# Optimization experiments

Measured on AMD Instinct MI355X. Metric: run time of the kernel, lower is better.

Reference implementation:

```python
import jax, jax.numpy as jnp
import numpy as np

N, D_IN, D_OUT = 8192, 4096, 4096
ACT_BITS = 8


def setup_inputs() -> dict:
    key = jax.random.key(0)
    k1, k2, k3 = jax.random.split(key, 3)
    x = jax.random.normal(k1, (N, D_IN), dtype=jnp.float32)
    # ternary weight buffer in {-1, 0, +1} (stored as int8 in torch; int32 here)
    weight = jax.random.randint(k2, (D_OUT, D_IN), -1, 2, dtype=jnp.int32)
    weight_scale = jnp.array(0.05, dtype=jnp.float32)
    bias = jax.random.normal(k3, (D_OUT,), dtype=jnp.float32) * 0.01
    return {"x": x, "weight": weight, "weight_scale": weight_scale, "bias": bias}


def reference(x, weight, weight_scale, bias):
    qmax = 2.0 ** (ACT_BITS - 1) - 1.0   # 127
    qmin = -(2.0 ** (ACT_BITS - 1))      # -128
    # absmax activation quantization (eval-mode path of the module)
    scale = jnp.max(jnp.abs(x)) / qmax
    scale = jnp.where(scale == 0, jnp.float32(1.0), scale)
    x_int = jnp.clip(jnp.round(x / scale), qmin, qmax)
    # ternary matmul: pos_mask - neg_mask == weight itself for ternary values,
    # so F.linear(x, pos) - F.linear(x, neg) == x @ W^T
    w = weight.astype(jnp.float32)
    out = x_int @ w.T  # [N, D_OUT]
    out = out * weight_scale * scale
    return out + bias
```

## Files before the change

kernel.cpp:

```cpp
#include <hip/hip_runtime.h>
#include <hip/hip_bf16.h>

#define M_DIM 8192
#define N_DIM 4096
#define K_DIM 4096

typedef __attribute__((ext_vector_type(4))) int int4v;

__device__ __forceinline__ int quant4(float4 v, float rs) {
    float r0 = rintf(v.x * rs), r1 = rintf(v.y * rs);
    float r2 = rintf(v.z * rs), r3 = rintf(v.w * rs);
    int i0 = (int)fminf(127.0f, fmaxf(-128.0f, r0));
    int i1 = (int)fminf(127.0f, fmaxf(-128.0f, r1));
    int i2 = (int)fminf(127.0f, fmaxf(-128.0f, r2));
    int i3 = (int)fminf(127.0f, fmaxf(-128.0f, r3));
    return (i0 & 255) | ((i1 & 255) << 8) | ((i2 & 255) << 16) | (i3 << 24);
}

__device__ __forceinline__ int pack4i(int4 v) {
    return (v.x & 255) | ((v.y & 255) << 8) | ((v.z & 255) << 16) | (v.w << 24);
}

#define WCVT_BLOCKS 1024
#define ABS_BLOCKS 2048
__global__ void prep1_kernel(const float4* __restrict__ x,
                             const int4* __restrict__ w,
                             int* __restrict__ wq,
                             unsigned* __restrict__ amax) {
    if (blockIdx.x < WCVT_BLOCKS) {
        const int t = WCVT_BLOCKS * 256;
        const int n = (N_DIM * K_DIM) / 4;
        for (int i = blockIdx.x * 256 + threadIdx.x; i < n; i += 4 * t) {
            int4 a = w[i], b = w[i + t], c = w[i + 2 * t], d = w[i + 3 * t];
            wq[i] = pack4i(a);
            wq[i + t] = pack4i(b);
            wq[i + 2 * t] = pack4i(c);
            wq[i + 3 * t] = pack4i(d);
        }
    } else {
        const int t = ABS_BLOCKS * 256;
        const int n = (M_DIM * K_DIM) / 4;
        float m = 0.0f;
        for (int i = (blockIdx.x - WCVT_BLOCKS) * 256 + threadIdx.x; i < n;
             i += 4 * t) {
            float4 a = x[i], b = x[i + t], c = x[i + 2 * t], d = x[i + 3 * t];
            float ma = fmaxf(fmaxf(fabsf(a.x), fabsf(a.y)), fmaxf(fabsf(a.z), fabsf(a.w)));
            float mb = fmaxf(fmaxf(fabsf(b.x), fabsf(b.y)), fmaxf(fabsf(b.z), fabsf(b.w)));
            float mc = fmaxf(fmaxf(fabsf(c.x), fabsf(c.y)), fmaxf(fabsf(c.z), fabsf(c.w)));
            float md = fmaxf(fmaxf(fabsf(d.x), fabsf(d.y)), fmaxf(fabsf(d.z), fabsf(d.w)));
            m = fmaxf(m, fmaxf(fmaxf(ma, mb), fmaxf(mc, md)));
        }
        #pragma unroll
        for (int off = 32; off > 0; off >>= 1)
            m = fmaxf(m, __shfl_down(m, off, 64));
        __shared__ float sm[4];
        if ((threadIdx.x & 63) == 0) sm[threadIdx.x >> 6] = m;
        __syncthreads();
        if (threadIdx.x == 0) {
            float b = fmaxf(fmaxf(sm[0], sm[1]), fmaxf(sm[2], sm[3]));
            atomicMax(amax, __float_as_uint(b));
        }
    }
}

#define QUANT_BLOCKS 2048
__global__ void quant_kernel(const float4* __restrict__ x, int* __restrict__ q,
                             const unsigned* __restrict__ amax_u) {
    float amax = __uint_as_float(*amax_u);
    float scale = amax * (1.0f / 127.0f);
    if (scale == 0.0f) scale = 1.0f;
    const float rs = 1.0f / scale;
    const int t = QUANT_BLOCKS * 256;
    const int n = (M_DIM * K_DIM) / 4;
    for (int i = blockIdx.x * 256 + threadIdx.x; i < n; i += 4 * t) {
        float4 a = x[i], b = x[i + t], c = x[i + 2 * t], d = x[i + 3 * t];
        q[i] = quant4(a, rs);
        q[i + t] = quant4(b, rs);
        q[i + 2 * t] = quant4(c, rs);
        q[i + 3 * t] = quant4(d, rs);
    }
}

__device__ __forceinline__ void gload16(const char* g, char* l) {
    __builtin_amdgcn_global_load_lds(
        (const __attribute__((address_space(1))) unsigned int*)g,
        (__attribute__((address_space(3))) unsigned int*)l,
        16, 0, 0);
}

#define FENCE() asm volatile("" ::: "memory")
#define BAR()                                \
    do {                                     \
        FENCE();                             \
        __builtin_amdgcn_s_barrier();        \
        FENCE();                             \
    } while (0)

__global__ __launch_bounds__(512, 2) void gemm_i8(
    const char* __restrict__ A,
    const char* __restrict__ B,
    float* __restrict__ C,
    const float* __restrict__ bias,
    const float* __restrict__ wscale,
    const unsigned* __restrict__ amax_u) {
    __shared__ __align__(16) char L[4][32768];

    const int f = blockIdx.x;
    const int xcd = f & 7;
    const int slot = f >> 3;
    const int sm = slot >> 3;
    int sn = slot & 7;
    if (sm & 1) sn = 7 - sn;
    const int mBase = ((xcd >> 1) * 8 + sm) * 256;
    const int nBase = ((xcd & 1) * 8 + sn) * 256;

    const int t = threadIdx.x;
    const int w = t >> 6;
    const int l = t & 63;
    const int lm = l & 15;
    const int lq = l >> 4;
    const int wm = w >> 2;
    const int wn = w & 3;

    const char* gp[4];
    int lo[4];
    #pragma unroll
    for (int p = 0; p < 4; ++p) {
        const int idx = p * 8 + w;
        if (idx < 16) {
            gp[p] = A + (size_t)(mBase + idx * 16 + lm) * K_DIM + lq * 16;
            lo[p] = idx * 1024;
        } else {
            gp[p] = B + (size_t)(nBase + (idx - 16) * 16 + lm) * K_DIM + lq * 16;
            lo[p] = 16384 + (idx - 16) * 1024;
        }
    }

    #define STG(tt, p) gload16(gp[p] + (size_t)(tt) * 64, &L[(tt) & 3][0] + lo[p])

    #pragma unroll
    for (int tt = 0; tt < 3; ++tt) {
        STG(tt, 0);
        STG(tt, 1);
        STG(tt, 2);
        STG(tt, 3);
    }

    int4v acc[8][4];
    #pragma unroll
    for (int r = 0; r < 8; ++r)
        #pragma unroll
        for (int c = 0; c < 4; ++c)
            acc[r][c] = (int4v){0, 0, 0, 0};

    asm volatile("s_waitcnt vmcnt(8)" ::: "memory");
    BAR();

    #define KTILE(u, DO_STAGE, VMSTR)                                           \
    do {                                                                        \
        const char* lb = &L[(u) & 3][0];                                        \
        const char* aB = lb + wm * 8192 + l * 16;                               \
        const char* bB = lb + 16384 + wn * 4096 + l * 16;                       \
        int4v af[4], bf[4];                                                     \
                      \
        _Pragma("unroll")                                                       \
        for (int r = 0; r < 4; ++r) af[r] = *(const int4v*)(aB + r * 1024);     \
        _Pragma("unroll")                                                       \
        for (int c = 0; c < 4; ++c) bf[c] = *(const int4v*)(bB + c * 1024);     \
        if (DO_STAGE) { STG((u) + 3, 0); STG((u) + 3, 1); }                     \
        BAR();                                                                  \
        __builtin_amdgcn_s_setprio(1);                                          \
        _Pragma("unroll")                                                       \
        for (int r = 0; r < 4; ++r)                                             \
            _Pragma("unroll")                                                   \
            for (int c = 0; c < 4; ++c)                                         \
                acc[r][c] = __builtin_amdgcn_mfma_i32_16x16x64_i8(              \
                    af[r], bf[c], acc[r][c], 0, 0, 0);                          \
        __builtin_amdgcn_s_setprio(0);                                          \
        BAR();                                                                  \
                                              \
        _Pragma("unroll")                                                       \
        for (int r = 0; r < 4; ++r)                                             \
            af[r] = *(const int4v*)(aB + (4 + r) * 1024);                       \
        if (DO_STAGE) { STG((u) + 3, 2); STG((u) + 3, 3); }                     \
        asm volatile("s_waitcnt " VMSTR ::: "memory");                          \
        BAR();                                                                  \
        __builtin_amdgcn_s_setprio(1);                                          \
        _Pragma("unroll")                                                       \
        for (int r = 0; r < 4; ++r)                                             \
            _Pragma("unroll")                                                   \
            for (int c = 0; c < 4; ++c)                                         \
                acc[4 + r][c] = __builtin_amdgcn_mfma_i32_16x16x64_i8(          \
                    af[r], bf[c], acc[4 + r][c], 0, 0, 0);                      \
        __builtin_amdgcn_s_setprio(0);                                          \
        BAR();                                                                  \
    } while (0)

    #pragma unroll 1
    for (int u = 0; u < 61; ++u) {
        KTILE(u, true, "vmcnt(8)");
    }
    KTILE(61, false, "vmcnt(4)");
    KTILE(62, false, "vmcnt(0)");
    KTILE(63, false, "vmcnt(0)");

    #undef KTILE
    #undef STG

    float amax = __uint_as_float(*amax_u);
    float scale = amax * (1.0f / 127.0f);
    if (scale == 0.0f) scale = 1.0f;
    const float s = wscale[0] * scale;

    #pragma unroll
    for (int ct = 0; ct < 4; ++ct) {
        const int col = nBase + wn * 64 + ct * 16 + lm;
        const float bb = bias[col];
        #pragma unroll
        for (int rt = 0; rt < 8; ++rt) {
            const int row0 = mBase + wm * 128 + rt * 16 + lq * 4;
            #pragma unroll
            for (int r = 0; r < 4; ++r) {
                C[(size_t)(row0 + r) * N_DIM + col] = (float)acc[rt][ct][r] * s + bb;
            }
        }
    }
}

extern "C" void kernel_launch(void* const* d_in, const int* in_sizes, int n_in,
                              void* d_out, int out_size, void* d_ws, size_t ws_size,
                              hipStream_t stream) {
    const float* x      = (const float*)d_in[0];
    const int* weight   = (const int*)d_in[1];
    const float* wscale = (const float*)d_in[2];
    const float* bias   = (const float*)d_in[3];
    float* out          = (float*)d_out;

    unsigned char* ws = (unsigned char*)d_ws;
    unsigned* amax = (unsigned*)ws;
    char* Aq = (char*)(ws + 256);
    char* Wb = (char*)(ws + 256 + (size_t)M_DIM * K_DIM);

    hipMemsetAsync(amax, 0, sizeof(unsigned), stream);

    prep1_kernel<<<WCVT_BLOCKS + ABS_BLOCKS, 256, 0, stream>>>(
        (const float4*)x, (const int4*)weight, (int*)Wb, amax);
    quant_kernel<<<QUANT_BLOCKS, 256, 0, stream>>>((const float4*)x, (int*)Aq, amax);

    gemm_i8<<<512, 512, 0, stream>>>(Aq, Wb, out, bias, wscale, amax);
}
```

Baseline: 437.7 us.

## Double-buffer LDS fragment registers to prefetch next k-tile during MFMA

Adds a two-slot register buffer for the A and B MFMA fragments. The first-half fragments of the next k-tile are read from LDS while the current tile's second-half MFMAs run, and the waitcnt placement and tail handling are restructured to match. The aim is to hide LDS read latency behind MFMA work. In exchange it raises VGPR pressure, which could reduce occupancy or cause spills.

Result: no change. 439.2 us (+0.3%).

```diff
diff --git a/kernel.cpp b/kernel.cpp
--- a/kernel.cpp
+++ b/kernel.cpp
@@ -156,18 +156,26 @@
     asm volatile("s_waitcnt vmcnt(8)" ::: "memory");
     BAR();
 
-    #define KTILE(u, DO_STAGE, VMSTR)                                           \
+    int4v afc[2][4], bfc[2][4], afh[4];
+    {
+        const char* lb = &L[0][0];
+        const char* aB = lb + wm * 8192 + l * 16;
+        const char* bB = lb + 16384 + wn * 4096 + l * 16;
+        #pragma unroll
+        for (int r = 0; r < 4; ++r) afc[0][r] = *(const int4v*)(aB + r * 1024);
+        #pragma unroll
+        for (int c = 0; c < 4; ++c) bfc[0][c] = *(const int4v*)(bB + c * 1024);
+    }
+
+    #define KTILE(u, P, WSTR, DOSTG, DORD)                                      \
     do {                                                                        \
         const char* lb = &L[(u) & 3][0];                                        \
         const char* aB = lb + wm * 8192 + l * 16;                               \
-        const char* bB = lb + 16384 + wn * 4096 + l * 16;                       \
-        int4v af[4], bf[4];                                                     \
-                      \
         _Pragma("unroll")                                                       \
-        for (int r = 0; r < 4; ++r) af[r] = *(const int4v*)(aB + r * 1024);     \
-        _Pragma("unroll")                                                       \
-        for (int c = 0; c < 4; ++c) bf[c] = *(const int4v*)(bB + c * 1024);     \
-        if (DO_STAGE) { STG((u) + 3, 0); STG((u) + 3, 1); }                     \
+        for (int r = 0; r < 4; ++r)                                             \
+            afh[r] = *(const int4v*)(aB + (4 + r) * 1024);                      \
+        if (DOSTG) { STG((u) + 3, 0); STG((u) + 3, 1); }                        \
+        asm volatile("s_waitcnt " WSTR ::: "memory");                           \
         BAR();                                                                  \
         __builtin_amdgcn_s_setprio(1);                                          \
         _Pragma("unroll")                                                       \
@@ -175,15 +183,21 @@
             _Pragma("unroll")                                                   \
             for (int c = 0; c < 4; ++c)                                         \
                 acc[r][c] = __builtin_amdgcn_mfma_i32_16x16x64_i8(              \
-                    af[r], bf[c], acc[r][c], 0, 0, 0);                          \
+                    afc[P][r], bfc[P][c], acc[r][c], 0, 0, 0);                  \
         __builtin_amdgcn_s_setprio(0);                                          \
         BAR();                                                                  \
-                                              \
-        _Pragma("unroll")                                                       \
-        for (int r = 0; r < 4; ++r)                                             \
-            af[r] = *(const int4v*)(aB + (4 + r) * 1024);                       \
-        if (DO_STAGE) { STG((u) + 3, 2); STG((u) + 3, 3); }                     \
-        asm volatile("s_waitcnt " VMSTR ::: "memory");                          \
+        if (DORD) {                                                             \
+            const char* lbN = &L[((u) + 1) & 3][0];                             \
+            const char* aN = lbN + wm * 8192 + l * 16;                          \
+            const char* bN = lbN + 16384 + wn * 4096 + l * 16;                  \
+            _Pragma("unroll")                                                   \
+            for (int r = 0; r < 4; ++r)                                         \
+                afc[(P) ^ 1][r] = *(const int4v*)(aN + r * 1024);               \
+            _Pragma("unroll")                                                   \
+            for (int c = 0; c < 4; ++c)                                         \
+                bfc[(P) ^ 1][c] = *(const int4v*)(bN + c * 1024);               \
+        }                                                                       \
+        if (DOSTG) { STG((u) + 3, 2); STG((u) + 3, 3); }                        \
         BAR();                                                                  \
         __builtin_amdgcn_s_setprio(1);                                          \
         _Pragma("unroll")                                                       \
@@ -191,18 +205,41 @@
             _Pragma("unroll")                                                   \
             for (int c = 0; c < 4; ++c)                                         \
                 acc[4 + r][c] = __builtin_amdgcn_mfma_i32_16x16x64_i8(          \
-                    af[r], bf[c], acc[4 + r][c], 0, 0, 0);                      \
+                    afh[r], bfc[P][c], acc[4 + r][c], 0, 0, 0);                 \
         __builtin_amdgcn_s_setprio(0);                                          \
         BAR();                                                                  \
     } while (0)
 
     #pragma unroll 1
-    for (int u = 0; u < 61; ++u) {
-        KTILE(u, true, "vmcnt(8)");
-    }
-    KTILE(61, false, "vmcnt(4)");
-    KTILE(62, false, "vmcnt(0)");
-    KTILE(63, false, "vmcnt(0)");
+    for (int u = 0; u < 60; u += 2) {
+        KTILE(u, 0, "vmcnt(6)", 1, 1);
+        KTILE(u + 1, 1, "vmcnt(6)", 1, 1);
+    }
+    KTILE(60, 0, "vmcnt(6)", 1, 1);
+    KTILE(61, 1, "vmcnt(4)", 0, 1);
+    KTILE(62, 0, "vmcnt(0)", 0, 1);
+    {
+        const char* lb = &L[63 & 3][0];
+        const char* aB = lb + wm * 8192 + l * 16;
+        #pragma unroll
+        for (int r = 0; r < 4; ++r)
+            afh[r] = *(const int4v*)(aB + (4 + r) * 1024);
+        BAR();
+        __builtin_amdgcn_s_setprio(1);
+        #pragma unroll
+        for (int r = 0; r < 4; ++r)
+            #pragma unroll
+            for (int c = 0; c < 4; ++c)
+                acc[r][c] = __builtin_amdgcn_mfma_i32_16x16x64_i8(
+                    afc[1][r], bfc[1][c], acc[r][c], 0, 0, 0);
+        #pragma unroll
+        for (int r = 0; r < 4; ++r)
+            #pragma unroll
+            for (int c = 0; c < 4; ++c)
+                acc[4 + r][c] = __builtin_amdgcn_mfma_i32_16x16x64_i8(
+                    afh[r], bfc[1][c], acc[4 + r][c], 0, 0, 0);
+        __builtin_amdgcn_s_setprio(0);
+    }
 
     #undef KTILE
     #undef STG
```
